# Performance work log

Hardware: AMD Instinct MI355X
Metric: run time of the kernel (lower is better)

Reference implementation:

```python
import jax, jax.numpy as jnp
import numpy as np
import math

B, T, D, H = 4, 2048, 1024, 16
DH = D // H


def setup_inputs() -> dict:
    key = jax.random.key(0)
    k1, k2, k3 = jax.random.split(key, 3)
    x = jax.random.normal(k1, (B, T, D), dtype=jnp.float32)
    # causal mask: True = masked (positions j > i)
    attn_mask = jnp.triu(jnp.ones((T, T), dtype=bool), k=1)
    key_padding_mask = jnp.zeros((B, T), dtype=bool)  # no padding
    W_qkv = jax.random.normal(k2, (D, 3 * D), dtype=jnp.float32) / math.sqrt(D)
    W_out = jax.random.normal(k3, (D, D), dtype=jnp.float32) / math.sqrt(D)
    return {"x": x, "W_qkv": W_qkv, "W_out": W_out,
            "attn_mask": attn_mask, "key_padding_mask": key_padding_mask}


def reference(x, W_qkv, W_out, attn_mask, key_padding_mask):
    # qkv projection (bias=False)
    qkv = x @ W_qkv                                   # [B,T,3D]
    q, k, v = jnp.split(qkv, 3, axis=-1)              # each [B,T,D]
    # reshape to heads: [B,H,T,DH]
    q = q.reshape(B, T, H, DH).transpose(0, 2, 1, 3)
    k = k.reshape(B, T, H, DH).transpose(0, 2, 1, 3)
    v = v.reshape(B, T, H, DH).transpose(0, 2, 1, 3)
    scale = 1.0 / math.sqrt(DH)
    scores = jnp.einsum('bhqd,bhkd->bhqk', q, k) * scale   # [B,H,T,T]
    neg_inf = jnp.float32(-jnp.inf)
    scores = jnp.where(attn_mask[None, None, :, :], neg_inf, scores)
    scores = jnp.where(key_padding_mask[:, None, None, :], neg_inf, scores)
    attn = jax.nn.softmax(scores, axis=-1)            # dropout p=0.0 -> identity
    out = jnp.einsum('bhqk,bhkd->bhqd', attn, v)      # [B,H,T,DH]
    out = out.transpose(0, 2, 1, 3).reshape(B, T, D)
    return out @ W_out
```

## Files before the change

### kernel.cpp

```cpp
#include <hip/hip_runtime.h>
#include <hip/hip_bf16.h>

#define Bsz 4
#define T 2048
#define D 1024
#define H 16
#define DH 64

typedef unsigned short u16;
typedef __attribute__((ext_vector_type(8))) __bf16 bf16x8;
typedef __attribute__((ext_vector_type(4))) float f32x4;

__device__ inline u16 f2bf(float f) {
  union { float f; unsigned u; } v; v.f = f;
  unsigned r = (v.u + 0x7FFFu + ((v.u >> 16) & 1u)) >> 16;
  return (u16)r;
}
__device__ inline unsigned pack_bf16(float a, float b) {
  union { float f; unsigned u; } A, B; A.f = a; B.f = b;
  unsigned au = A.u + 0x8000u, bu = B.u + 0x8000u;
  return __builtin_amdgcn_perm(bu, au, 0x07060302);
}

__device__ inline void gll16(const u16* g, u16* l) {
  __builtin_amdgcn_global_load_lds((const __attribute__((address_space(1))) void*)g,
                                   (__attribute__((address_space(3))) void*)l, 16, 0, 0);
}

__global__ __launch_bounds__(256) void convert_f32_bf16(const float* __restrict__ in,
                                                        u16* __restrict__ out, int n4) {
  int i = blockIdx.x * 256 + threadIdx.x;
  if (i < n4) {
    float4 v = reinterpret_cast<const float4*>(in)[i];
    ushort4 o;
    o.x = f2bf(v.x); o.y = f2bf(v.y); o.z = f2bf(v.z); o.w = f2bf(v.w);
    reinterpret_cast<ushort4*>(out)[i] = o;
  }
}

__global__ __launch_bounds__(256) void transpose_f32_bf16(const float* __restrict__ in,
                                                          u16* __restrict__ out, int K, int N) {
  __shared__ float tile[32][33];
  int tx = threadIdx.x & 31, ty = threadIdx.x >> 5;
  int n0 = blockIdx.x * 32, k0 = blockIdx.y * 32;
  #pragma unroll
  for (int i = 0; i < 4; ++i)
    tile[ty + i * 8][tx] = in[(size_t)(k0 + ty + i * 8) * N + n0 + tx];
  __syncthreads();
  #pragma unroll
  for (int i = 0; i < 4; ++i)
    out[(size_t)(n0 + ty + i * 8) * K + k0 + tx] = f2bf(tile[tx][ty + i * 8]);
}

template <int MODE>
__global__ __launch_bounds__(512, 2) void gemm256(const u16* __restrict__ A, const u16* __restrict__ BT,
                                                  float* __restrict__ C,
                                                  u16* __restrict__ Qh, u16* __restrict__ Kh,
                                                  u16* __restrict__ VTh, int M, int N, int K) {
  __shared__ alignas(16) u16 SA[2][256][64];
  __shared__ alignas(16) u16 SB[2][256][64];
  int tid = threadIdx.x;

  int flat = blockIdx.y * gridDim.x + blockIdx.x;
  int cpx = (int)(gridDim.x * gridDim.y) >> 3;
  int nf = (flat & 7) * cpx + (flat >> 3);
  int bx = nf % (int)gridDim.x, by = nf / (int)gridDim.x;
  int m0 = by * 256, n0 = bx * 256;

  int w = tid >> 6, lane = tid & 63;
  int llo = lane & 15, lhi = lane >> 4;
  int wr = w >> 2, wc = w & 3;

  int cs0 = ((lhi ^ (llo & 7)) << 3);
  int cs1 = (((4 + lhi) ^ (llo & 7)) << 3);

  int srcCol = (((lane & 7) ^ ((lane >> 3) & 7)) << 3);
  const u16* gAl = A + (size_t)(m0 + w * 8 + (lane >> 3)) * K + srcCol;
  const u16* gBl = BT + (size_t)(n0 + w * 8 + (lane >> 3)) * K + srcCol;

  f32x4 acc[8][4];
  #pragma unroll
  for (int i = 0; i < 8; ++i)
    #pragma unroll
    for (int j = 0; j < 4; ++j) acc[i][j] = (f32x4){0.f, 0.f, 0.f, 0.f};

  int nt = K >> 6;

  auto stA = [&](int buf, int h, int c, int kt) {
    gll16(gAl + (h * 128 + c * 64) * K + kt * 64, &SA[buf][h * 128 + c * 64 + w * 8][0]);
  };
  auto stB = [&](int buf, int h, int c, int kt) {
    gll16(gBl + (h * 128 + c * 64) * K + kt * 64, &SB[buf][h * 128 + c * 64 + w * 8][0]);
  };

  stA(0, 0, 0, 0); stA(0, 0, 1, 0); stA(0, 1, 0, 0); stA(0, 1, 1, 0);
  stB(0, 0, 0, 0); stB(0, 0, 1, 0); stB(0, 1, 0, 0); stB(0, 1, 1, 0);
  stB(1, 0, 0, 1); stB(1, 0, 1, 1);
  stA(1, 0, 0, 1); stA(1, 0, 1, 1);
  asm volatile("s_waitcnt vmcnt(4)" ::: "memory");
  __builtin_amdgcn_s_barrier();

  bf16x8 aA[4][2], bB[4][2];

  #pragma unroll 2
  for (int t = 0; t < nt; ++t) {
    int p = t & 1;

    #pragma unroll
    for (int i = 0; i < 4; ++i) {
      aA[i][0] = *reinterpret_cast<const bf16x8*>(&SA[p][wr * 128 + i * 16 + llo][cs0]);
      aA[i][1] = *reinterpret_cast<const bf16x8*>(&SA[p][wr * 128 + i * 16 + llo][cs1]);
    }
    #pragma unroll
    for (int j = 0; j < 2; ++j) {
      bB[j][0] = *reinterpret_cast<const bf16x8*>(&SB[p][wc * 64 + j * 16 + llo][cs0]);
      bB[j][1] = *reinterpret_cast<const bf16x8*>(&SB[p][wc * 64 + j * 16 + llo][cs1]);
    }
    if (t + 1 < nt) { stA(1 - p, 1, 0, t + 1); stA(1 - p, 1, 1, t + 1); }
    __builtin_amdgcn_s_barrier();
    __builtin_amdgcn_s_setprio(1);
    #pragma unroll
    for (int i = 0; i < 4; ++i)
      #pragma unroll
      for (int j = 0; j < 2; ++j) {
        acc[i][j] = __builtin_amdgcn_mfma_f32_16x16x32_bf16(aA[i][0], bB[j][0], acc[i][j], 0, 0, 0);
        acc[i][j] = __builtin_amdgcn_mfma_f32_16x16x32_bf16(aA[i][1], bB[j][1], acc[i][j], 0, 0, 0);
      }
    __builtin_amdgcn_s_setprio(0);
    __builtin_amdgcn_s_barrier();

    #pragma unroll
    for (int j = 2; j < 4; ++j) {
      bB[j][0] = *reinterpret_cast<const bf16x8*>(&SB[p][wc * 64 + j * 16 + llo][cs0]);
      bB[j][1] = *reinterpret_cast<const bf16x8*>(&SB[p][wc * 64 + j * 16 + llo][cs1]);
    }
    if (t + 1 < nt) { stB(1 - p, 1, 0, t + 1); stB(1 - p, 1, 1, t + 1); }
    __builtin_amdgcn_s_barrier();
    __builtin_amdgcn_s_setprio(1);
    #pragma unroll
    for (int i = 0; i < 4; ++i)
      #pragma unroll
      for (int j = 2; j < 4; ++j) {
        acc[i][j] = __builtin_amdgcn_mfma_f32_16x16x32_bf16(aA[i][0], bB[j][0], acc[i][j], 0, 0, 0);
        acc[i][j] = __builtin_amdgcn_mfma_f32_16x16x32_bf16(aA[i][1], bB[j][1], acc[i][j], 0, 0, 0);
      }
    __builtin_amdgcn_s_setprio(0);
    __builtin_amdgcn_s_barrier();

    #pragma unroll
    for (int i = 0; i < 4; ++i) {
      aA[i][0] = *reinterpret_cast<const bf16x8*>(&SA[p][wr * 128 + 64 + i * 16 + llo][cs0]);
      aA[i][1] = *reinterpret_cast<const bf16x8*>(&SA[p][wr * 128 + 64 + i * 16 + llo][cs1]);
    }
    if (t + 2 < nt) { stB(p, 0, 0, t + 2); stB(p, 0, 1, t + 2); }
    __builtin_amdgcn_s_barrier();
    __builtin_amdgcn_s_setprio(1);
    #pragma unroll
    for (int i = 0; i < 4; ++i)
      #pragma unroll
      for (int j = 0; j < 2; ++j) {
        acc[4 + i][j] = __builtin_amdgcn_mfma_f32_16x16x32_bf16(aA[i][0], bB[j][0], acc[4 + i][j], 0, 0, 0);
        acc[4 + i][j] = __builtin_amdgcn_mfma_f32_16x16x32_bf16(aA[i][1], bB[j][1], acc[4 + i][j], 0, 0, 0);
      }
    __builtin_amdgcn_s_setprio(0);
    __builtin_amdgcn_s_barrier();

    if (t + 2 < nt) { stA(p, 0, 0, t + 2); stA(p, 0, 1, t + 2); }
    __builtin_amdgcn_s_setprio(1);
    #pragma unroll
    for (int i = 0; i < 4; ++i)
      #pragma unroll
      for (int j = 2; j < 4; ++j) {
        acc[4 + i][j] = __builtin_amdgcn_mfma_f32_16x16x32_bf16(aA[i][0], bB[j][0], acc[4 + i][j], 0, 0, 0);
        acc[4 + i][j] = __builtin_amdgcn_mfma_f32_16x16x32_bf16(aA[i][1], bB[j][1], acc[4 + i][j], 0, 0, 0);
      }
    __builtin_amdgcn_s_setprio(0);
    if (t + 2 < nt)      asm volatile("s_waitcnt vmcnt(4)" ::: "memory");
    else if (t + 1 < nt) asm volatile("s_waitcnt vmcnt(0)" ::: "memory");
    __builtin_amdgcn_s_barrier();
  }

  if (MODE == 0) {
    #pragma unroll
    for (int i = 0; i < 8; ++i) {
      int ml = m0 + wr * 128 + i * 16 + lhi * 4;
      #pragma unroll
      for (int j = 0; j < 4; ++j) {
        int nl = n0 + wc * 64 + j * 16 + llo;
        #pragma unroll
        for (int r = 0; r < 4; ++r)
          C[(size_t)(ml + r) * N + nl] = acc[i][j][r];
      }
    }
  } else {
    int seg = n0 >> 10;
    #pragma unroll
    for (int i = 0; i < 8; ++i) {
      int mbase = m0 + wr * 128 + i * 16 + lhi * 4;
      int t0 = mbase & (T - 1);
      int b_ = mbase >> 11;
      #pragma unroll
      for (int j = 0; j < 4; ++j) {
        int nl = n0 + wc * 64 + j * 16 + llo;
        int h = (nl >> 6) & 15, d = nl & 63;
        int bh = b_ * H + h;
        if (seg == 0) {
          #pragma unroll
          for (int r = 0; r < 4; ++r)
            Qh[((size_t)bh * T + t0 + r) * DH + d] = f2bf(acc[i][j][r] * 0.125f);
        } else if (seg == 1) {
          #pragma unroll
          for (int r = 0; r < 4; ++r)
            Kh[((size_t)bh * T + t0 + r) * DH + d] = f2bf(acc[i][j][r]);
        } else {
          uint2 p;
          p.x = pack_bf16(acc[i][j][0], acc[i][j][1]);
          p.y = pack_bf16(acc[i][j][2], acc[i][j][3]);
          *reinterpret_cast<uint2*>(&VTh[((size_t)bh * DH + d) * T + t0]) = p;
        }
      }
    }
  }
}

template <int BN, int MODE>
__global__ __launch_bounds__(512, 4) void gemmX(const u16* __restrict__ A, const u16* __restrict__ BT,
                                                float* __restrict__ C,
                                                u16* __restrict__ Qh, u16* __restrict__ Kh,
                                                u16* __restrict__ VTh, int M, int N, int K) {
  constexpr int NB = BN / 64;
  __shared__ alignas(16) u16 SA[2][2][128][32];
  __shared__ alignas(16) u16 SB[2][2][BN][32];
  u16* sbFlat = &SB[0][0][0][0];
  int tid = threadIdx.x;

  int flat = blockIdx.y * gridDim.x + blockIdx.x;
  int cpx = (int)(gridDim.x * gridDim.y) >> 3;
  int nf = (flat & 7) * cpx + (flat >> 3);
  int bx = nf % (int)gridDim.x, by = nf / (int)gridDim.x;
  int m0 = by * 128, n0 = bx * BN;

  int w = tid >> 6, lane = tid & 63;
  int llo = lane & 15, lhi = lane >> 4;
  int wr = w >> 2, wc = w & 3;

  int cs = ((lhi ^ ((llo >> 1) & 3)) << 3);

  int rA = w * 16 + (lane >> 2);
  const u16* srcA = A + (size_t)(m0 + rA) * K + (((lane & 3) ^ ((rA >> 1) & 3)) << 3);
  const u16* srcB[NB];
  #pragma unroll
  for (int q = 0; q < NB; ++q) {
    int rr = q * 128 + w * 16 + (lane >> 2);
    int kB = (rr >= BN) ? 1 : 0;
    int rB = rr - kB * BN;
    srcB[q] = BT + (size_t)(n0 + rB) * K + kB * 32 + (((lane & 3) ^ ((rB >> 1) & 3)) << 3);
  }

  f32x4 acc[4][NB];
  #pragma unroll
  for (int i = 0; i < 4; ++i)
    #pragma unroll
    for (int j = 0; j < NB; ++j) acc[i][j] = (f32x4){0.f, 0.f, 0.f, 0.f};

  int nt = K >> 6;

  auto stage = [&](int g, int buf) {
    #pragma unroll
    for (int k = 0; k < 2; ++k)
      gll16(srcA + g * 64 + k * 32, &SA[buf][k][w * 16][0]);
    #pragma unroll
    for (int q = 0; q < NB; ++q)
      gll16(srcB[q] + g * 64, sbFlat + (size_t)buf * (2 * BN * 32) + (q * 128 + w * 16) * 32);
  };

  stage(0, 0);
  asm volatile("s_waitcnt vmcnt(0)" ::: "memory");
  __builtin_amdgcn_s_barrier();

  #pragma unroll 2
  for (int g = 0; g < nt; ++g) {
    int p = g & 1;
    if (g + 1 < nt) stage(g + 1, 1 - p);

    #pragma unroll
    for (int k = 0; k < 2; ++k) {
      bf16x8 aA[4], bB[NB];
      #pragma unroll
      for (int i = 0; i < 4; ++i)
        aA[i] = *reinterpret_cast<const bf16x8*>(&SA[p][k][wr * 64 + i * 16 + llo][cs]);
      #pragma unroll
      for (int j = 0; j < NB; ++j)
        bB[j] = *reinterpret_cast<const bf16x8*>(&SB[p][k][wc * (BN / 4) + j * 16 + llo][cs]);
      __builtin_amdgcn_s_setprio(1);
      #pragma unroll
      for (int i = 0; i < 4; ++i)
        #pragma unroll
        for (int j = 0; j < NB; ++j)
          acc[i][j] = __builtin_amdgcn_mfma_f32_16x16x32_bf16(aA[i], bB[j], acc[i][j], 0, 0, 0);
      __builtin_amdgcn_s_setprio(0);
    }

    asm volatile("s_waitcnt vmcnt(0)" ::: "memory");
    __builtin_amdgcn_s_barrier();
  }

  if (MODE == 0) {
    #pragma unroll
    for (int i = 0; i < 4; ++i) {
      int ml = m0 + wr * 64 + i * 16 + lhi * 4;
      #pragma unroll
      for (int j = 0; j < NB; ++j) {
        int nl = n0 + wc * (BN / 4) + j * 16 + llo;
        #pragma unroll
        for (int r = 0; r < 4; ++r)
          C[(size_t)(ml + r) * N + nl] = acc[i][j][r];
      }
    }
  } else {
    #pragma unroll
    for (int i = 0; i < 4; ++i) {
      int mbase = m0 + wr * 64 + i * 16 + lhi * 4;
      int t0 = mbase & (T - 1);
      int b_ = mbase >> 11;
      #pragma unroll
      for (int j = 0; j < NB; ++j) {
        int ncol0 = n0 + wc * (BN / 4) + j * 16;
        int seg = ncol0 >> 10;
        int nl = ncol0 + llo;
        int h = (nl >> 6) & 15, d = nl & 63;
        int bh = b_ * H + h;
        if (seg == 0) {
          #pragma unroll
          for (int r = 0; r < 4; ++r)
            Qh[((size_t)bh * T + t0 + r) * DH + d] = f2bf(acc[i][j][r] * 0.125f);
        } else if (seg == 1) {
          #pragma unroll
          for (int r = 0; r < 4; ++r)
            Kh[((size_t)bh * T + t0 + r) * DH + d] = f2bf(acc[i][j][r]);
        } else {
          uint2 pk;
          pk.x = pack_bf16(acc[i][j][0], acc[i][j][1]);
          pk.y = pack_bf16(acc[i][j][2], acc[i][j][3]);
          *reinterpret_cast<uint2*>(&VTh[((size_t)bh * DH + d) * T + t0]) = pk;
        }
      }
    }
  }
}

__global__ __launch_bounds__(512, 4) void attn_fwd(const u16* __restrict__ Qh, const u16* __restrict__ Kh,
                                                   const u16* __restrict__ VTh, u16* __restrict__ AO) {
  __shared__ u16 QP[8][16][64];
  __shared__ u16 Ks[64][64];
  __shared__ u16 Vs[64][64];
  int tid = threadIdx.x;
  int qp = blockIdx.x, bh = blockIdx.y;
  int w = tid >> 6, lane = tid & 63;
  int llo = lane & 15, lhi = lane >> 4;
  int swz = llo & 7;

  int qrow_s = tid >> 2, qc = tid & 3;
  int krow_s = tid >> 3, kc = tid & 7;
  int kvcol = ((kc ^ (krow_s & 7)) << 3);
  const u16* kbase = Kh + ((size_t)bh * T + krow_s) * DH + kc * 8;
  const u16* vbase = VTh + ((size_t)bh * DH + krow_s) * T + kc * 8;
  int b = bh >> 4, h = bh & 15;

  #pragma unroll 1
  for (int half = 0; half < 2; ++half) {
    int qt = half ? (15 - qp) : qp;
    int q0 = qt * 128;

    bf16x8 aq[2];
    {
      const uint4* g = reinterpret_cast<const uint4*>(
          Qh + ((size_t)bh * T + q0 + qrow_s) * DH + qc * 16);
      uint4 a = g[0], bb = g[1];
      int r7 = qrow_s & 7;
      *reinterpret_cast<uint4*>(&QP[w][qrow_s & 15][((2 * qc) ^ r7) << 3]) = a;
      *reinterpret_cast<uint4*>(&QP[w][qrow_s & 15][((2 * qc + 1) ^ r7) << 3]) = bb;
      #pragma unroll
      for (int ks = 0; ks < 2; ++ks)
        aq[ks] = *reinterpret_cast<const bf16x8*>(&QP[w][llo][((ks * 4 + lhi) ^ swz) << 3]);
    }

    f32x4 o[4];
    #pragma unroll
    for (int i = 0; i < 4; ++i) o[i] = (f32x4){0.f, 0.f, 0.f, 0.f};
    float l_run = 0.f;

    int nj = 2 * qt + 2;
    uint4 ka = *reinterpret_cast<const uint4*>(kbase);
    uint4 va = *reinterpret_cast<const uint4*>(vbase);

    #pragma unroll 1
    for (int j = 0; j < nj; ++j) {
      __syncthreads();
      *reinterpret_cast<uint4*>(&Ks[krow_s][kvcol]) = ka;
      *reinterpret_cast<uint4*>(&Vs[krow_s][kvcol]) = va;
      if (j + 1 < nj) {
        ka = *reinterpret_cast<const uint4*>(kbase + (size_t)(j + 1) * 64 * DH);
        va = *reinterpret_cast<const uint4*>(vbase + (j + 1) * 64);
      } else if (half == 0) {
        ka = *reinterpret_cast<const uint4*>(kbase);
        va = *reinterpret_cast<const uint4*>(vbase);
      }
      __syncthreads();

      if (q0 + w * 16 + 15 >= j * 64) {
        f32x4 sc[4];
        #pragma unroll
        for (int kt = 0; kt < 4; ++kt) {
          bf16x8 bk0 = *reinterpret_cast<const bf16x8*>(&Ks[kt * 16 + llo][(lhi ^ swz) << 3]);
          bf16x8 bk1 = *reinterpret_cast<const bf16x8*>(&Ks[kt * 16 + llo][((4 + lhi) ^ swz) << 3]);
          f32x4 z = (f32x4){0.f, 0.f, 0.f, 0.f};
          f32x4 t0 = __builtin_amdgcn_mfma_f32_16x16x32_bf16(bk0, aq[0], z, 0, 0, 0);
          sc[kt] = __builtin_amdgcn_mfma_f32_16x16x32_bf16(bk1, aq[1], t0, 0, 0, 0);
        }

        if (j >= 2 * qt) {
          int qrow_g = q0 + w * 16 + llo;
          #pragma unroll
          for (int kt = 0; kt < 4; ++kt)
            #pragma unroll
            for (int r = 0; r < 4; ++r) {
              int key_g = j * 64 + kt * 16 + lhi * 4 + r;
              if (key_g > qrow_g) sc[kt][r] = -__builtin_inff();
            }
        }

        float s_sum = 0.f;
        #pragma unroll
        for (int kt = 0; kt < 4; ++kt)
          #pragma unroll
          for (int r = 0; r < 4; ++r) {
            float p = __expf(sc[kt][r]);
            sc[kt][r] = p;
            s_sum += p;
          }
        s_sum += __shfl_xor(s_sum, 16);
        s_sum += __shfl_xor(s_sum, 32);
        l_run += s_sum;

        #pragma unroll
        for (int kt = 0; kt < 4; ++kt) {
          uint2 p;
          p.x = pack_bf16(sc[kt][0], sc[kt][1]);
          p.y = pack_bf16(sc[kt][2], sc[kt][3]);
          *reinterpret_cast<uint2*>(
              &QP[w][llo][(((2 * kt + (lhi >> 1)) ^ swz) << 3) + (lhi & 1) * 4]) = p;
        }

        #pragma unroll
        for (int kk2 = 0; kk2 < 2; ++kk2) {
          bf16x8 pa = *reinterpret_cast<const bf16x8*>(&QP[w][llo][((kk2 * 4 + lhi) ^ swz) << 3]);
          #pragma unroll
          for (int nt = 0; nt < 4; ++nt) {
            bf16x8 bv = *reinterpret_cast<const bf16x8*>(&Vs[nt * 16 + llo][((kk2 * 4 + lhi) ^ swz) << 3]);
            o[nt] = __builtin_amdgcn_mfma_f32_16x16x32_bf16(pa, bv, o[nt], 0, 0, 0);
          }
        }
      }
    }

    #pragma unroll
    for (int r = 0; r < 4; ++r) {
      float inv = 1.f / __shfl(l_run, lhi * 4 + r);
      int t = q0 + w * 16 + lhi * 4 + r;
      #pragma unroll
      for (int nt = 0; nt < 4; ++nt)
        AO[((size_t)(b * T + t)) * D + h * 64 + nt * 16 + llo] = f2bf(o[nt][r] * inv);
    }
  }
}

extern "C" void kernel_launch(void* const* d_in, const int* in_sizes, int n_in,
                              void* d_out, int out_size, void* d_ws, size_t ws_size,
                              hipStream_t stream) {
  (void)in_sizes; (void)n_in; (void)out_size;
  const float* x = (const float*)d_in[0];
  const float* Wqkv = (const float*)d_in[1];
  const float* Wout = (const float*)d_in[2];
  float* out = (float*)d_out;

  char* ws = (char*)d_ws;
  size_t off = 0;
  u16* xb = (u16*)(ws + off);    off += (size_t)Bsz * T * D * 2;
  u16* WqkvT = (u16*)(ws + off); off += (size_t)3 * D * D * 2;
  u16* WoutT = (u16*)(ws + off); off += (size_t)D * D * 2;
  u16* Qh = (u16*)(ws + off);    off += (size_t)Bsz * H * T * DH * 2;
  u16* Kh = (u16*)(ws + off);    off += (size_t)Bsz * H * T * DH * 2;
  u16* VTh = (u16*)(ws + off);   off += (size_t)Bsz * H * DH * T * 2;
  u16* AO = xb;
  if (ws_size < off) return;

  int n4 = Bsz * T * D / 4;
  convert_f32_bf16<<<(n4 + 255) / 256, 256, 0, stream>>>(x, xb, n4);
  transpose_f32_bf16<<<dim3(3 * D / 32, D / 32), 256, 0, stream>>>(Wqkv, WqkvT, D, 3 * D);
  transpose_f32_bf16<<<dim3(D / 32, D / 32), 256, 0, stream>>>(Wout, WoutT, D, D);
  gemm256<1><<<dim3(3 * D / 256, Bsz * T / 256), 512, 0, stream>>>(xb, WqkvT, nullptr, Qh, Kh, VTh,
                                                                   Bsz * T, 3 * D, D);
  attn_fwd<<<dim3(8, Bsz * H), 512, 0, stream>>>(Qh, Kh, VTh, AO);
  gemmX<128, 0><<<dim3(D / 128, Bsz * T / 128), 512, 0, stream>>>(AO, WoutT, out, nullptr, nullptr, nullptr,
                                                                  Bsz * T, D, D);
}
```

Measured before the change: 255.2 us.

## Use 256x192 QKV GEMM tiles and 32-row-per-wave attention with 256 threads

The QKV projection GEMM switches from 256x256 to 256x192 tiles. That gives 16x32=512 blocks instead of 12x32=384, so the work spreads more evenly over the CUs. Its prefetch schedule moves from a two-tile-ahead pattern to a single-tile-ahead pattern with new vmcnt waits. The attention kernel drops to 256 threads, with each wave handling 32 query rows through two MFMA row groups, so each K/V tile loaded into LDS is reused across more queries per wave. The costs are higher register pressure, fewer waves for latency hiding, and a reworked, riskier load/wait schedule in the GEMM.

```diff
diff --git a/kernel.cpp b/kernel.cpp
--- a/kernel.cpp
+++ b/kernel.cpp
@@ -58,14 +58,14 @@
                                                   u16* __restrict__ Qh, u16* __restrict__ Kh,
                                                   u16* __restrict__ VTh, int M, int N, int K) {
   __shared__ alignas(16) u16 SA[2][256][64];
-  __shared__ alignas(16) u16 SB[2][256][64];
+  __shared__ alignas(16) u16 SB[2][192][64];
   int tid = threadIdx.x;
 
   int flat = blockIdx.y * gridDim.x + blockIdx.x;
   int cpx = (int)(gridDim.x * gridDim.y) >> 3;
   int nf = (flat & 7) * cpx + (flat >> 3);
   int bx = nf % (int)gridDim.x, by = nf / (int)gridDim.x;
-  int m0 = by * 256, n0 = bx * 256;
+  int m0 = by * 256, n0 = bx * 192;
 
   int w = tid >> 6, lane = tid & 63;
   int llo = lane & 15, lhi = lane >> 4;
@@ -78,29 +78,27 @@
   const u16* gAl = A + (size_t)(m0 + w * 8 + (lane >> 3)) * K + srcCol;
   const u16* gBl = BT + (size_t)(n0 + w * 8 + (lane >> 3)) * K + srcCol;
 
-  f32x4 acc[8][4];
+  f32x4 acc[8][3];
   #pragma unroll
   for (int i = 0; i < 8; ++i)
     #pragma unroll
-    for (int j = 0; j < 4; ++j) acc[i][j] = (f32x4){0.f, 0.f, 0.f, 0.f};
+    for (int j = 0; j < 3; ++j) acc[i][j] = (f32x4){0.f, 0.f, 0.f, 0.f};
 
   int nt = K >> 6;
 
-  auto stA = [&](int buf, int h, int c, int kt) {
-    gll16(gAl + (h * 128 + c * 64) * K + kt * 64, &SA[buf][h * 128 + c * 64 + w * 8][0]);
+  auto stA = [&](int buf, int c, int kt) {
+    gll16(gAl + (size_t)(c * 64) * K + kt * 64, &SA[buf][c * 64 + w * 8][0]);
   };
-  auto stB = [&](int buf, int h, int c, int kt) {
-    gll16(gBl + (h * 128 + c * 64) * K + kt * 64, &SB[buf][h * 128 + c * 64 + w * 8][0]);
+  auto stB = [&](int buf, int c, int kt) {
+    gll16(gBl + (size_t)(c * 64) * K + kt * 64, &SB[buf][c * 64 + w * 8][0]);
   };
 
-  stA(0, 0, 0, 0); stA(0, 0, 1, 0); stA(0, 1, 0, 0); stA(0, 1, 1, 0);
-  stB(0, 0, 0, 0); stB(0, 0, 1, 0); stB(0, 1, 0, 0); stB(0, 1, 1, 0);
-  stB(1, 0, 0, 1); stB(1, 0, 1, 1);
-  stA(1, 0, 0, 1); stA(1, 0, 1, 1);
-  asm volatile("s_waitcnt vmcnt(4)" ::: "memory");
+  stA(0, 0, 0); stA(0, 1, 0); stA(0, 2, 0); stA(0, 3, 0);
+  stB(0, 0, 0); stB(0, 1, 0); stB(0, 2, 0);
+  asm volatile("s_waitcnt vmcnt(0)" ::: "memory");
   __builtin_amdgcn_s_barrier();
 
-  bf16x8 aA[4][2], bB[4][2];
+  bf16x8 aA[4][2], bB[3][2];
 
   #pragma unroll 2
   for (int t = 0; t < nt; ++t) {
@@ -113,10 +111,10 @@
     }
     #pragma unroll
     for (int j = 0; j < 2; ++j) {
-      bB[j][0] = *reinterpret_cast<const bf16x8*>(&SB[p][wc * 64 + j * 16 + llo][cs0]);
-      bB[j][1] = *reinterpret_cast<const bf16x8*>(&SB[p][wc * 64 + j * 16 + llo][cs1]);
-    }
-    if (t + 1 < nt) { stA(1 - p, 1, 0, t + 1); stA(1 - p, 1, 1, t + 1); }
+      bB[j][0] = *reinterpret_cast<const bf16x8*>(&SB[p][wc * 48 + j * 16 + llo][cs0]);
+      bB[j][1] = *reinterpret_cast<const bf16x8*>(&SB[p][wc * 48 + j * 16 + llo][cs1]);
+    }
+    if (t + 1 < nt) { stA(1 - p, 0, t + 1); stA(1 - p, 2, t + 1); }
     __builtin_amdgcn_s_barrier();
     __builtin_amdgcn_s_setprio(1);
     #pragma unroll
@@ -129,22 +127,19 @@
     __builtin_amdgcn_s_setprio(0);
     __builtin_amdgcn_s_barrier();
 
-    #pragma unroll
-    for (int j = 2; j < 4; ++j) {
-      bB[j][0] = *reinterpret_cast<const bf16x8*>(&SB[p][wc * 64 + j * 16 + llo][cs0]);
-      bB[j][1] = *reinterpret_cast<const bf16x8*>(&SB[p][wc * 64 + j * 16 + llo][cs1]);
-    }
-    if (t + 1 < nt) { stB(1 - p, 1, 0, t + 1); stB(1 - p, 1, 1, t + 1); }
+    bB[2][0] = *reinterpret_cast<const bf16x8*>(&SB[p][wc * 48 + 32 + llo][cs0]);
+    bB[2][1] = *reinterpret_cast<const bf16x8*>(&SB[p][wc * 48 + 32 + llo][cs1]);
+    if (t + 1 < nt) { stB(1 - p, 0, t + 1); stB(1 - p, 1, t + 1); }
     __builtin_amdgcn_s_barrier();
     __builtin_amdgcn_s_setprio(1);
     #pragma unroll
-    for (int i = 0; i < 4; ++i)
-      #pragma unroll
-      for (int j = 2; j < 4; ++j) {
-        acc[i][j] = __builtin_amdgcn_mfma_f32_16x16x32_bf16(aA[i][0], bB[j][0], acc[i][j], 0, 0, 0);
-        acc[i][j] = __builtin_amdgcn_mfma_f32_16x16x32_bf16(aA[i][1], bB[j][1], acc[i][j], 0, 0, 0);
-      }
+    for (int i = 0; i < 4; ++i) {
+      acc[i][2] = __builtin_amdgcn_mfma_f32_16x16x32_bf16(aA[i][0], bB[2][0], acc[i][2], 0, 0, 0);
+      acc[i][2] = __builtin_amdgcn_mfma_f32_16x16x32_bf16(aA[i][1], bB[2][1], acc[i][2], 0, 0, 0);
+    }
     __builtin_amdgcn_s_setprio(0);
+    if (t + 1 < nt) asm volatile("s_waitcnt vmcnt(4)" ::: "memory");
+    else            asm volatile("s_waitcnt vmcnt(0)" ::: "memory");
     __builtin_amdgcn_s_barrier();
 
     #pragma unroll
@@ -152,7 +147,7 @@
       aA[i][0] = *reinterpret_cast<const bf16x8*>(&SA[p][wr * 128 + 64 + i * 16 + llo][cs0]);
       aA[i][1] = *reinterpret_cast<const bf16x8*>(&SA[p][wr * 128 + 64 + i * 16 + llo][cs1]);
     }
-    if (t + 2 < nt) { stB(p, 0, 0, t + 2); stB(p, 0, 1, t + 2); }
+    if (t + 1 < nt) { stB(1 - p, 2, t + 1); stA(1 - p, 1, t + 1); }
     __builtin_amdgcn_s_barrier();
     __builtin_amdgcn_s_setprio(1);
     #pragma unroll
@@ -165,18 +160,15 @@
     __builtin_amdgcn_s_setprio(0);
     __builtin_amdgcn_s_barrier();
 
-    if (t + 2 < nt) { stA(p, 0, 0, t + 2); stA(p, 0, 1, t + 2); }
+    if (t + 1 < nt) stA(1 - p, 3, t + 1);
     __builtin_amdgcn_s_setprio(1);
     #pragma unroll
-    for (int i = 0; i < 4; ++i)
-      #pragma unroll
-      for (int j = 2; j < 4; ++j) {
-        acc[4 + i][j] = __builtin_amdgcn_mfma_f32_16x16x32_bf16(aA[i][0], bB[j][0], acc[4 + i][j], 0, 0, 0);
-        acc[4 + i][j] = __builtin_amdgcn_mfma_f32_16x16x32_bf16(aA[i][1], bB[j][1], acc[4 + i][j], 0, 0, 0);
-      }
+    for (int i = 0; i < 4; ++i) {
+      acc[4 + i][2] = __builtin_amdgcn_mfma_f32_16x16x32_bf16(aA[i][0], bB[2][0], acc[4 + i][2], 0, 0, 0);
+      acc[4 + i][2] = __builtin_amdgcn_mfma_f32_16x16x32_bf16(aA[i][1], bB[2][1], acc[4 + i][2], 0, 0, 0);
+    }
     __builtin_amdgcn_s_setprio(0);
-    if (t + 2 < nt)      asm volatile("s_waitcnt vmcnt(4)" ::: "memory");
-    else if (t + 1 < nt) asm volatile("s_waitcnt vmcnt(0)" ::: "memory");
+    if (t + 1 < nt) asm volatile("s_waitcnt vmcnt(2)" ::: "memory");
     __builtin_amdgcn_s_barrier();
   }
 
@@ -185,23 +177,23 @@
     for (int i = 0; i < 8; ++i) {
       int ml = m0 + wr * 128 + i * 16 + lhi * 4;
       #pragma unroll
-      for (int j = 0; j < 4; ++j) {
-        int nl = n0 + wc * 64 + j * 16 + llo;
+      for (int j = 0; j < 3; ++j) {
+        int nl = n0 + wc * 48 + j * 16 + llo;
         #pragma unroll
         for (int r = 0; r < 4; ++r)
           C[(size_t)(ml + r) * N + nl] = acc[i][j][r];
       }
     }
   } else {
-    int seg = n0 >> 10;
     #pragma unroll
     for (int i = 0; i < 8; ++i) {
       int mbase = m0 + wr * 128 + i * 16 + lhi * 4;
       int t0 = mbase & (T - 1);
       int b_ = mbase >> 11;
       #pragma unroll
-      for (int j = 0; j < 4; ++j) {
-        int nl = n0 + wc * 64 + j * 16 + llo;
+      for (int j = 0; j < 3; ++j) {
+        int nl = n0 + wc * 48 + j * 16 + llo;
+        int seg = (n0 + wc * 48 + j * 16) >> 10;
         int h = (nl >> 6) & 15, d = nl & 63;
         int bh = b_ * H + h;
         if (seg == 0) {
@@ -349,9 +341,9 @@
   }
 }
 
-__global__ __launch_bounds__(512, 4) void attn_fwd(const u16* __restrict__ Qh, const u16* __restrict__ Kh,
+__global__ __launch_bounds__(256, 2) void attn_fwd(const u16* __restrict__ Qh, const u16* __restrict__ Kh,
                                                    const u16* __restrict__ VTh, u16* __restrict__ AO) {
-  __shared__ u16 QP[8][16][64];
+  __shared__ u16 QP[4][32][64];
   __shared__ u16 Ks[64][64];
   __shared__ u16 Vs[64][64];
   int tid = threadIdx.x;
@@ -360,7 +352,7 @@
   int llo = lane & 15, lhi = lane >> 4;
   int swz = llo & 7;
 
-  int qrow_s = tid >> 2, qc = tid & 3;
+  int qrow_s = tid >> 1, qc = tid & 1;
   int krow_s = tid >> 3, kc = tid & 7;
   int kvcol = ((kc ^ (krow_s & 7)) << 3);
   const u16* kbase = Kh + ((size_t)bh * T + krow_s) * DH + kc * 8;
@@ -372,93 +364,119 @@
     int qt = half ? (15 - qp) : qp;
     int q0 = qt * 128;
 
-    bf16x8 aq[2];
+    bf16x8 aq0[2], aq1[2];
     {
       const uint4* g = reinterpret_cast<const uint4*>(
-          Qh + ((size_t)bh * T + q0 + qrow_s) * DH + qc * 16);
-      uint4 a = g[0], bb = g[1];
+          Qh + ((size_t)bh * T + q0 + qrow_s) * DH + qc * 32);
+      uint4 g0 = g[0], g1 = g[1], g2 = g[2], g3 = g[3];
       int r7 = qrow_s & 7;
-      *reinterpret_cast<uint4*>(&QP[w][qrow_s & 15][((2 * qc) ^ r7) << 3]) = a;
-      *reinterpret_cast<uint4*>(&QP[w][qrow_s & 15][((2 * qc + 1) ^ r7) << 3]) = bb;
-      #pragma unroll
-      for (int ks = 0; ks < 2; ++ks)
-        aq[ks] = *reinterpret_cast<const bf16x8*>(&QP[w][llo][((ks * 4 + lhi) ^ swz) << 3]);
-    }
-
-    f32x4 o[4];
-    #pragma unroll
-    for (int i = 0; i < 4; ++i) o[i] = (f32x4){0.f, 0.f, 0.f, 0.f};
-    float l_run = 0.f;
+      int rr = qrow_s & 31;
+      *reinterpret_cast<uint4*>(&QP[w][rr][((qc * 4 + 0) ^ r7) << 3]) = g0;
+      *reinterpret_cast<uint4*>(&QP[w][rr][((qc * 4 + 1) ^ r7) << 3]) = g1;
+      *reinterpret_cast<uint4*>(&QP[w][rr][((qc * 4 + 2) ^ r7) << 3]) = g2;
+      *reinterpret_cast<uint4*>(&QP[w][rr][((qc * 4 + 3) ^ r7) << 3]) = g3;
+      #pragma unroll
+      for (int ks = 0; ks < 2; ++ks) {
+        aq0[ks] = *reinterpret_cast<const bf16x8*>(&QP[w][llo][((ks * 4 + lhi) ^ swz) << 3]);
+        aq1[ks] = *reinterpret_cast<const bf16x8*>(&QP[w][16 + llo][((ks * 4 + lhi) ^ swz) << 3]);
+      }
+    }
+
+    f32x4 o0[4], o1[4];
+    #pragma unroll
+    for (int i = 0; i < 4; ++i) {
+      o0[i] = (f32x4){0.f, 0.f, 0.f, 0.f};
+      o1[i] = (f32x4){0.f, 0.f, 0.f, 0.f};
+    }
+    float l0 = 0.f, l1 = 0.f;
 
     int nj = 2 * qt + 2;
-    uint4 ka = *reinterpret_cast<const uint4*>(kbase);
-    uint4 va = *reinterpret_cast<const uint4*>(vbase);
+    uint4 ka0 = *reinterpret_cast<const uint4*>(kbase);
+    uint4 ka1 = *reinterpret_cast<const uint4*>(kbase + 32 * DH);
+    uint4 va0 = *reinterpret_cast<const uint4*>(vbase);
+    uint4 va1 = *reinterpret_cast<const uint4*>(vbase + 32 * T);
 
     #pragma unroll 1
     for (int j = 0; j < nj; ++j) {
       __syncthreads();
-      *reinterpret_cast<uint4*>(&Ks[krow_s][kvcol]) = ka;
-      *reinterpret_cast<uint4*>(&Vs[krow_s][kvcol]) = va;
+      *reinterpret_cast<uint4*>(&Ks[krow_s][kvcol]) = ka0;
+      *reinterpret_cast<uint4*>(&Ks[krow_s + 32][kvcol]) = ka1;
+      *reinterpret_cast<uint4*>(&Vs[krow_s][kvcol]) = va0;
+      *reinterpret_cast<uint4*>(&Vs[krow_s + 32][kvcol]) = va1;
       if (j + 1 < nj) {
-        ka = *reinterpret_cast<const uint4*>(kbase + (size_t)(j + 1) * 64 * DH);
-        va = *reinterpret_cast<const uint4*>(vbase + (j + 1) * 64);
+        ka0 = *reinterpret_cast<const uint4*>(kbase + (size_t)(j + 1) * 64 * DH);
+        ka1 = *reinterpret_cast<const uint4*>(kbase + (size_t)(j + 1) * 64 * DH + 32 * DH);
+        va0 = *reinterpret_cast<const uint4*>(vbase + (j + 1) * 64);
+        va1 = *reinterpret_cast<const uint4*>(vbase + 32 * T + (j + 1) * 64);
       } else if (half == 0) {
-        ka = *reinterpret_cast<const uint4*>(kbase);
-        va = *reinterpret_cast<const uint4*>(vbase);
+        ka0 = *reinterpret_cast<const uint4*>(kbase);
+        ka1 = *reinterpret_cast<const uint4*>(kbase + 32 * DH);
+        va0 = *reinterpret_cast<const uint4*>(vbase);
+        va1 = *reinterpret_cast<const uint4*>(vbase + 32 * T);
       }
       __syncthreads();
 
-      if (q0 + w * 16 + 15 >= j * 64) {
-        f32x4 sc[4];
+      if (q0 + w * 32 + 31 >= j * 64) {
+        f32x4 sc0[4], sc1[4];
         #pragma unroll
         for (int kt = 0; kt < 4; ++kt) {
           bf16x8 bk0 = *reinterpret_cast<const bf16x8*>(&Ks[kt * 16 + llo][(lhi ^ swz) << 3]);
           bf16x8 bk1 = *reinterpret_cast<const bf16x8*>(&Ks[kt * 16 + llo][((4 + lhi) ^ swz) << 3]);
           f32x4 z = (f32x4){0.f, 0.f, 0.f, 0.f};
-          f32x4 t0 = __builtin_amdgcn_mfma_f32_16x16x32_bf16(bk0, aq[0], z, 0, 0, 0);
-          sc[kt] = __builtin_amdgcn_mfma_f32_16x16x32_bf16(bk1, aq[1], t0, 0, 0, 0);
+          f32x4 t00 = __builtin_amdgcn_mfma_f32_16x16x32_bf16(bk0, aq0[0], z, 0, 0, 0);
+          sc0[kt] = __builtin_amdgcn_mfma_f32_16x16x32_bf16(bk1, aq0[1], t00, 0, 0, 0);
+          f32x4 t01 = __builtin_amdgcn_mfma_f32_16x16x32_bf16(bk0, aq1[0], z, 0, 0, 0);
+          sc1[kt] = __builtin_amdgcn_mfma_f32_16x16x32_bf16(bk1, aq1[1], t01, 0, 0, 0);
         }
 
         if (j >= 2 * qt) {
-          int qrow_g = q0 + w * 16 + llo;
+          int qg0 = q0 + w * 32 + llo;
+          int qg1 = qg0 + 16;
           #pragma unroll
           for (int kt = 0; kt < 4; ++kt)
             #pragma unroll
             for (int r = 0; r < 4; ++r) {
               int key_g = j * 64 + kt * 16 + lhi * 4 + r;
-              if (key_g > qrow_g) sc[kt][r] = -__builtin_inff();
+              if (key_g > qg0) sc0[kt][r] = -__builtin_inff();
+              if (key_g > qg1) sc1[kt][r] = -__builtin_inff();
             }
         }
 
-        float s_sum = 0.f;
+        float s0 = 0.f, s1 = 0.f;
         #pragma unroll
         for (int kt = 0; kt < 4; ++kt)
           #pragma unroll
           for (int r = 0; r < 4; ++r) {
-            float p = __expf(sc[kt][r]);
-            sc[kt][r] = p;
-            s_sum += p;
+            float p0 = __expf(sc0[kt][r]);
+            float p1 = __expf(sc1[kt][r]);
+            sc0[kt][r] = p0; sc1[kt][r] = p1;
+            s0 += p0; s1 += p1;
           }
-        s_sum += __shfl_xor(s_sum, 16);
-        s_sum += __shfl_xor(s_sum, 32);
-        l_run += s_sum;
+        s0 += __shfl_xor(s0, 16); s0 += __shfl_xor(s0, 32); l0 += s0;
+        s1 += __shfl_xor(s1, 16); s1 += __shfl_xor(s1, 32); l1 += s1;
 
         #pragma unroll
         for (int kt = 0; kt < 4; ++kt) {
-          uint2 p;
-          p.x = pack_bf16(sc[kt][0], sc[kt][1]);
-          p.y = pack_bf16(sc[kt][2], sc[kt][3]);
-          *reinterpret_cast<uint2*>(
-              &QP[w][llo][(((2 * kt + (lhi >> 1)) ^ swz) << 3) + (lhi & 1) * 4]) = p;
+          uint2 p0, p1;
+          p0.x = pack_bf16(sc0[kt][0], sc0[kt][1]);
+          p0.y = pack_bf16(sc0[kt][2], sc0[kt][3]);
+          p1.x = pack_bf16(sc1[kt][0], sc1[kt][1]);
+          p1.y = pack_bf16(sc1[kt][2], sc1[kt][3]);
+          int col = (((2 * kt + (lhi >> 1)) ^ swz) << 3) + (lhi & 1) * 4;
+          *reinterpret_cast<uint2*>(&QP[w][llo][col]) = p0;
+          *reinterpret_cast<uint2*>(&QP[w][16 + llo][col]) = p1;
         }
 
         #pragma unroll
         for (int kk2 = 0; kk2 < 2; ++kk2) {
-          bf16x8 pa = *reinterpret_cast<const bf16x8*>(&QP[w][llo][((kk2 * 4 + lhi) ^ swz) << 3]);
+          int pcol = ((kk2 * 4 + lhi) ^ swz) << 3;
+          bf16x8 pa0 = *reinterpret_cast<const bf16x8*>(&QP[w][llo][pcol]);
+          bf16x8 pa1 = *reinterpret_cast<const bf16x8*>(&QP[w][16 + llo][pcol]);
           #pragma unroll
           for (int nt = 0; nt < 4; ++nt) {
-            bf16x8 bv = *reinterpret_cast<const bf16x8*>(&Vs[nt * 16 + llo][((kk2 * 4 + lhi) ^ swz) << 3]);
-            o[nt] = __builtin_amdgcn_mfma_f32_16x16x32_bf16(pa, bv, o[nt], 0, 0, 0);
+            bf16x8 bv = *reinterpret_cast<const bf16x8*>(&Vs[nt * 16 + llo][pcol]);
+            o0[nt] = __builtin_amdgcn_mfma_f32_16x16x32_bf16(pa0, bv, o0[nt], 0, 0, 0);
+            o1[nt] = __builtin_amdgcn_mfma_f32_16x16x32_bf16(pa1, bv, o1[nt], 0, 0, 0);
           }
         }
       }
@@ -466,11 +484,15 @@
 
     #pragma unroll
     for (int r = 0; r < 4; ++r) {
-      float inv = 1.f / __shfl(l_run, lhi * 4 + r);
-      int t = q0 + w * 16 + lhi * 4 + r;
-      #pragma unroll
-      for (int nt = 0; nt < 4; ++nt)
-        AO[((size_t)(b * T + t)) * D + h * 64 + nt * 16 + llo] = f2bf(o[nt][r] * inv);
+      float inv0 = 1.f / __shfl(l0, lhi * 4 + r);
+      float inv1 = 1.f / __shfl(l1, lhi * 4 + r);
+      int t0_ = q0 + w * 32 + lhi * 4 + r;
+      int t1_ = t0_ + 16;
+      #pragma unroll
+      for (int nt = 0; nt < 4; ++nt) {
+        AO[((size_t)(b * T + t0_)) * D + h * 64 + nt * 16 + llo] = f2bf(o0[nt][r] * inv0);
+        AO[((size_t)(b * T + t1_)) * D + h * 64 + nt * 16 + llo] = f2bf(o1[nt][r] * inv1);
+      }
     }
   }
 }
@@ -499,9 +521,9 @@
   convert_f32_bf16<<<(n4 + 255) / 256, 256, 0, stream>>>(x, xb, n4);
   transpose_f32_bf16<<<dim3(3 * D / 32, D / 32), 256, 0, stream>>>(Wqkv, WqkvT, D, 3 * D);
   transpose_f32_bf16<<<dim3(D / 32, D / 32), 256, 0, stream>>>(Wout, WoutT, D, D);
-  gemm256<1><<<dim3(3 * D / 256, Bsz * T / 256), 512, 0, stream>>>(xb, WqkvT, nullptr, Qh, Kh, VTh,
+  gemm256<1><<<dim3(3 * D / 192, Bsz * T / 256), 512, 0, stream>>>(xb, WqkvT, nullptr, Qh, Kh, VTh,
                                                                    Bsz * T, 3 * D, D);
-  attn_fwd<<<dim3(8, Bsz * H), 512, 0, stream>>>(Qh, Kh, VTh, AO);
+  attn_fwd<<<dim3(8, Bsz * H), 256, 0, stream>>>(Qh, Kh, VTh, AO);
   gemmX<128, 0><<<dim3(D / 128, Bsz * T / 128), 512, 0, stream>>>(AO, WoutT, out, nullptr, nullptr, nullptr,
                                                                   Bsz * T, D, D);
 }
```

Result: no change. 252.8 us (-0.9%).
